# Optimization experiments

Measured on AMD Instinct MI355X. Metric: run time of the kernel, lower is better.

## Reference

```python
import jax, jax.numpy as jnp
import numpy as np

B, T, D = 8, 2048, 2048


def setup_inputs() -> dict:
    key = jax.random.key(0)
    ks = jax.random.split(key, 6)
    s = 1.0 / np.sqrt(D)
    return {
        "x": jax.random.normal(ks[0], (B, T, D), dtype=jnp.float32),
        "h_prev": jax.random.normal(ks[1], (B, D), dtype=jnp.float32),
        "Wz": jax.random.uniform(ks[2], (D, D), minval=-s, maxval=s, dtype=jnp.float32),
        "bz": jax.random.uniform(ks[3], (D,), minval=-s, maxval=s, dtype=jnp.float32),
        "Wh": jax.random.uniform(ks[4], (D, D), minval=-s, maxval=s, dtype=jnp.float32),
        "bh": jax.random.uniform(ks[5], (D,), minval=-s, maxval=s, dtype=jnp.float32),
    }


def reference(x, h_prev, Wz, bz, Wh, bh):
    # Batched projections over all timesteps (torch Linear: x @ W.T + b)
    z = jax.nn.sigmoid(jnp.einsum('btd,ed->bte', x, Wz) + bz)  # [B,T,D]
    h_tilde = jnp.einsum('btd,ed->bte', x, Wh) + bh            # [B,T,D]
    # Recurrence h_t = a_t * h_{t-1} + b_t as a parallel associative scan
    a = 1.0 - z
    b = z * h_tilde

    def combine(l, r):
        al, bl = l
        ar, br = r
        return (al * ar, ar * bl + br)

    a_cum, b_cum = jax.lax.associative_scan(combine, (a, b), axis=1)
    out = b_cum + a_cum * h_prev[:, None, :]  # add contribution of initial state
    return out, out[:, -1, :]
```

## Files before the change

### kernel.cpp

```cpp
#include <hip/hip_runtime.h>
#include <hip/hip_bf16.h>
#include <cstdint>

typedef __bf16 bf16_t;
typedef __attribute__((ext_vector_type(8))) __bf16 bf16x8;
typedef __attribute__((ext_vector_type(4))) __bf16 bf16x4;
typedef __attribute__((ext_vector_type(4))) float f32x4;

#define B_ 8
#define T_ 2048
#define D_ 2048
#define M_ (B_ * T_)
#define N2_ (2 * D_)
#define K_ D_
#define NT (K_ / 64)

#define NC 32
#define CHUNK (T_ / NC)

#define BAR() __builtin_amdgcn_s_barrier()
#define WAIT_LGKM0() asm volatile("s_waitcnt lgkmcnt(0)" ::: "memory")
#define WAIT_VM(n) asm volatile("s_waitcnt vmcnt(" #n ")" ::: "memory")


__global__ void conv_x_kernel(const float4* __restrict__ in, bf16x4* __restrict__ out, int n4) {
    int i = blockIdx.x * blockDim.x + threadIdx.x;
    if (i >= n4) return;
    float4 v = in[i];
    bf16x4 o = { (bf16_t)v.x, (bf16_t)v.y, (bf16_t)v.z, (bf16_t)v.w };
    out[i] = o;
}

__global__ void conv_w_kernel(const float4* __restrict__ Wz, const float4* __restrict__ Wh,
                              bf16x4* __restrict__ Wb, int n4, int d4) {
    int i = blockIdx.x * blockDim.x + threadIdx.x;
    if (i >= n4) return;
    int row = i / d4;
    int c = i - row * d4;
    float4 vz = Wz[i];
    float4 vh = Wh[i];
    bf16x4 oz = { (bf16_t)vz.x, (bf16_t)vz.y, (bf16_t)vz.z, (bf16_t)vz.w };
    bf16x4 oh = { (bf16_t)vh.x, (bf16_t)vh.y, (bf16_t)vh.z, (bf16_t)vh.w };
    Wb[(size_t)(2 * row) * d4 + c] = oz;
    Wb[(size_t)(2 * row + 1) * d4 + c] = oh;
}


__device__ __forceinline__ void gload_lds16(const bf16_t* g, char* l) {
    __builtin_amdgcn_global_load_lds(
        (__attribute__((address_space(1))) void*)(g),
        (__attribute__((address_space(3))) void*)(l), 16, 0, 0);
}


__global__ __launch_bounds__(512, 2) void gemm_fused(
    const bf16_t* __restrict__ Xb,
    const bf16_t* __restrict__ Wb,
    const float* __restrict__ bz, const float* __restrict__ bh,
    bf16_t* __restrict__ Aco,
    bf16_t* __restrict__ Bco)
{
    __shared__ __attribute__((aligned(16))) char lds[131072];

    const int t = threadIdx.x;
    const int wave = t >> 6, lane = t & 63;
    const int wr = wave >> 2, wc = wave & 3;
    const int fr = lane & 15, ln4 = lane >> 4;
    const int fr7 = fr & 7;
    const int bn0 = blockIdx.x * 256;
    const int bm0 = blockIdx.y * 256;

    const int l3 = lane >> 3, l7 = lane & 7;
    const int schunk = (l7 ^ l3) * 8;
    const int srow = wave * 8 + l3;

    const int csA[2] = { ((0 + ln4) ^ fr7) * 16, ((4 + ln4) ^ fr7) * 16 };
    const int rbaseA = wr * 16384 + fr * 128;
    const int rbaseB = wc * 8192 + fr * 128;

    auto stageA = [&](int buf, int h, int u) {
        const bf16_t* g = Xb + (size_t)(bm0 + h * 128 + srow) * K_ + u * 64 + schunk;
        char* l0 = lds + buf * 65536 + h * 16384 + wave * 1024;
        gload_lds16(g, l0);
        gload_lds16(g + (size_t)64 * K_, l0 + 8192);
    };
    auto stageB = [&](int buf, int h, int u) {
        const bf16_t* g = Wb + (size_t)(bn0 + h * 128 + srow) * K_ + u * 64 + schunk;
        char* l0 = lds + buf * 65536 + 32768 + h * 16384 + wave * 1024;
        gload_lds16(g, l0);
        gload_lds16(g + (size_t)64 * K_, l0 + 8192);
    };

#define RD_A(p, mi, kh) (*(const bf16x8*)(lds + (p) * 65536 + rbaseA + (mi) * 2048 + csA[kh]))
#define RD_B(p, ni, kh) (*(const bf16x8*)(lds + (p) * 65536 + 32768 + rbaseB + (ni) * 2048 + csA[kh]))

    f32x4 acc[8][4] = {};
    bf16x8 afr[4][2], bfr[4][2];

    stageA(0, 0, 0); stageA(0, 1, 0); stageB(0, 0, 0); stageB(0, 1, 0);
    stageA(1, 0, 1); stageA(1, 1, 1);
    WAIT_VM(4);
    BAR();

    for (int u = 0; u < NT; ++u) {
        const int p = u & 1;

#pragma unroll
        for (int mi = 0; mi < 4; ++mi)
#pragma unroll
            for (int kh = 0; kh < 2; ++kh)
                afr[mi][kh] = RD_A(p, mi, kh);
#pragma unroll
        for (int ni = 0; ni < 2; ++ni)
#pragma unroll
            for (int kh = 0; kh < 2; ++kh)
                bfr[ni][kh] = RD_B(p, ni, kh);
        if (u + 1 < NT) stageB(p ^ 1, 0, u + 1);
        BAR();
        __builtin_amdgcn_s_setprio(1);
#pragma unroll
        for (int mi = 0; mi < 4; ++mi)
#pragma unroll
            for (int ni = 0; ni < 2; ++ni)
#pragma unroll
                for (int kh = 0; kh < 2; ++kh)
                    acc[mi][ni] = __builtin_amdgcn_mfma_f32_16x16x32_bf16(
                        afr[mi][kh], bfr[ni][kh], acc[mi][ni], 0, 0, 0);
        __builtin_amdgcn_s_setprio(0);
        BAR();

#pragma unroll
        for (int ni = 2; ni < 4; ++ni)
#pragma unroll
            for (int kh = 0; kh < 2; ++kh)
                bfr[ni][kh] = RD_B(p, ni, kh);
        if (u + 1 < NT) stageB(p ^ 1, 1, u + 1);
        BAR();
        __builtin_amdgcn_s_setprio(1);
#pragma unroll
        for (int mi = 0; mi < 4; ++mi)
#pragma unroll
            for (int ni = 2; ni < 4; ++ni)
#pragma unroll
                for (int kh = 0; kh < 2; ++kh)
                    acc[mi][ni] = __builtin_amdgcn_mfma_f32_16x16x32_bf16(
                        afr[mi][kh], bfr[ni][kh], acc[mi][ni], 0, 0, 0);
        __builtin_amdgcn_s_setprio(0);
        BAR();

#pragma unroll
        for (int mi = 0; mi < 4; ++mi)
#pragma unroll
            for (int kh = 0; kh < 2; ++kh)
                afr[mi][kh] = RD_A(p, mi + 4, kh);
        WAIT_LGKM0();
        BAR();
        if (u + 2 < NT) stageA(p, 0, u + 2);
        __builtin_amdgcn_s_setprio(1);
#pragma unroll
        for (int mi = 0; mi < 4; ++mi)
#pragma unroll
            for (int ni = 0; ni < 2; ++ni)
#pragma unroll
                for (int kh = 0; kh < 2; ++kh)
                    acc[mi + 4][ni] = __builtin_amdgcn_mfma_f32_16x16x32_bf16(
                        afr[mi][kh], bfr[ni][kh], acc[mi + 4][ni], 0, 0, 0);
        __builtin_amdgcn_s_setprio(0);
        BAR();

        if (u + 2 < NT) stageA(p, 1, u + 2);
        __builtin_amdgcn_s_setprio(1);
#pragma unroll
        for (int mi = 0; mi < 4; ++mi)
#pragma unroll
            for (int ni = 2; ni < 4; ++ni)
#pragma unroll
                for (int kh = 0; kh < 2; ++kh)
                    acc[mi + 4][ni] = __builtin_amdgcn_mfma_f32_16x16x32_bf16(
                        afr[mi][kh], bfr[ni][kh], acc[mi + 4][ni], 0, 0, 0);
        __builtin_amdgcn_s_setprio(0);
        if (u < NT - 2)       { WAIT_VM(4); }
        else if (u == NT - 2) { WAIT_VM(0); }
        BAR();
    }

    float bzv[4], bhv[4];
#pragma unroll
    for (int ni = 0; ni < 4; ++ni) {
        int ch = (bn0 + wc * 64 + ni * 16 + fr) >> 1;
        bzv[ni] = bz[ch];
        bhv[ni] = bh[ch];
    }
#pragma unroll
    for (int mi = 0; mi < 8; ++mi) {
#pragma unroll
        for (int ni = 0; ni < 4; ++ni) {
#pragma unroll
            for (int q = 0; q < 4; ++q) {
                float v = acc[mi][ni][q];
                float other = __shfl_xor(v, 1);
                int m = bm0 + wr * 128 + mi * 16 + ln4 * 4 + q;
                int n2 = bn0 + wc * 64 + ni * 16 + fr;
                int ch = n2 >> 1;
                float zraw = (lane & 1) ? other : v;
                float z = 1.0f / (1.0f + __expf(-(zraw + bzv[ni])));
                if (lane & 1) {
                    Bco[(size_t)m * D_ + ch] = (bf16_t)(z * (v + bhv[ni]));
                } else {
                    Aco[(size_t)m * D_ + ch] = (bf16_t)(1.0f - z);
                }
            }
        }
    }
}


__global__ void scan_chunk_summary(const bf16_t* __restrict__ Aco, const bf16_t* __restrict__ Bco,
                                   float* __restrict__ cA, float* __restrict__ cB) {
    int d = blockIdx.x * blockDim.x + threadIdx.x;
    int c = blockIdx.y, bb = blockIdx.z;
    size_t base = ((size_t)bb * T_ + (size_t)c * CHUNK) * D_ + d;
    float A = 1.0f, Bv = 0.0f;
#pragma unroll 4
    for (int tt = 0; tt < CHUNK; ++tt) {
        float a = (float)Aco[base + (size_t)tt * D_];
        float b = (float)Bco[base + (size_t)tt * D_];
        A *= a;
        Bv = a * Bv + b;
    }
    size_t ci = ((size_t)bb * NC + c) * D_ + d;
    cA[ci] = A;
    cB[ci] = Bv;
}

__global__ void scan_carry(const float* __restrict__ cA, const float* __restrict__ cB,
                           const float* __restrict__ h_prev, float* __restrict__ carry) {
    int idx = blockIdx.x * blockDim.x + threadIdx.x;
    int bb = idx / D_, d = idx - bb * D_;
    float h = h_prev[idx];
    for (int c = 0; c < NC; ++c) {
        size_t ci = ((size_t)bb * NC + c) * D_ + d;
        carry[ci] = h;
        h = cA[ci] * h + cB[ci];
    }
}

__global__ void scan_apply(const bf16_t* __restrict__ Aco, const bf16_t* __restrict__ Bco,
                           const float* __restrict__ carry, float* __restrict__ out,
                           float* __restrict__ last) {
    int d = blockIdx.x * blockDim.x + threadIdx.x;
    int c = blockIdx.y, bb = blockIdx.z;
    size_t ci = ((size_t)bb * NC + c) * D_ + d;
    float h = carry[ci];
    size_t base = ((size_t)bb * T_ + (size_t)c * CHUNK) * D_ + d;
    for (int tt = 0; tt < CHUNK; ++tt) {
        float a = (float)Aco[base + (size_t)tt * D_];
        float b = (float)Bco[base + (size_t)tt * D_];
        h = a * h + b;
        out[base + (size_t)tt * D_] = h;
    }
    if (c == NC - 1) last[(size_t)bb * D_ + d] = h;
}


extern "C" void kernel_launch(void* const* d_in, const int* in_sizes, int n_in,
                              void* d_out, int out_size, void* d_ws, size_t ws_size,
                              hipStream_t stream) {
    const float* x      = (const float*)d_in[0];
    const float* h_prev = (const float*)d_in[1];
    const float* Wz     = (const float*)d_in[2];
    const float* bz     = (const float*)d_in[3];
    const float* Wh     = (const float*)d_in[4];
    const float* bh     = (const float*)d_in[5];

    float* out  = (float*)d_out;
    float* last = out + (size_t)M_ * D_;

    char* ws = (char*)d_ws;
    bf16_t* Xb  = (bf16_t*)ws;
    bf16_t* Wb  = (bf16_t*)(ws + (size_t)M_ * K_ * 2);
    bf16_t* Aco = (bf16_t*)((char*)Wb + (size_t)N2_ * K_ * 2);
    bf16_t* Bco = Aco + (size_t)M_ * D_;
    float*  cA  = (float*)((char*)Bco + (size_t)M_ * D_ * 2);
    float*  cB  = cA + (size_t)B_ * NC * D_;
    float*  carry = cB + (size_t)B_ * NC * D_;

    {
        int n4 = M_ * K_ / 4;
        conv_x_kernel<<<(n4 + 255) / 256, 256, 0, stream>>>((const float4*)x, (bf16x4*)Xb, n4);
    }
    {
        int n4 = D_ * D_ / 4;
        conv_w_kernel<<<(n4 + 255) / 256, 256, 0, stream>>>((const float4*)Wz, (const float4*)Wh,
                                                            (bf16x4*)Wb, n4, D_ / 4);
    }
    gemm_fused<<<dim3(N2_ / 256, M_ / 256), 512, 0, stream>>>(Xb, Wb, bz, bh, Aco, Bco);
    scan_chunk_summary<<<dim3(D_ / 256, NC, B_), 256, 0, stream>>>(Aco, Bco, cA, cB);
    scan_carry<<<(B_ * D_) / 256, 256, 0, stream>>>(cA, cB, h_prev, carry);
    scan_apply<<<dim3(D_ / 256, NC, B_), 256, 0, stream>>>(Aco, Bco, carry, out, last);
}
```

Before: 596.6 us.

## Interleave gate coefficients into packed words and fold carry scan into apply

The GEMM epilogue now writes the a and b coefficients as one packed 32-bit word (two bf16 values) per element instead of two separate bf16 arrays. Each scan kernel can then fetch both values with a single load. The separate scan_carry kernel is removed, and each apply block instead recomputes its starting carry by walking the earlier chunk summaries, which saves a launch and a round trip through memory at the cost of redundant serial work. Unroll factors in the scan loops are also raised.

```diff
diff --git a/kernel.cpp b/kernel.cpp
--- a/kernel.cpp
+++ b/kernel.cpp
@@ -1,6 +1,7 @@
 #include <hip/hip_runtime.h>
 #include <hip/hip_bf16.h>
 #include <cstdint>
+#include <cstring>
 
 typedef __bf16 bf16_t;
 typedef __attribute__((ext_vector_type(8))) __bf16 bf16x8;
@@ -21,6 +22,13 @@
 #define BAR() __builtin_amdgcn_s_barrier()
 #define WAIT_LGKM0() asm volatile("s_waitcnt lgkmcnt(0)" ::: "memory")
 #define WAIT_VM(n) asm volatile("s_waitcnt vmcnt(" #n ")" ::: "memory")
+
+__device__ __forceinline__ float bfbits_to_f(uint32_t u16) {
+    uint32_t u = u16 << 16;
+    float f;
+    memcpy(&f, &u, 4);
+    return f;
+}
 
 
 __global__ void conv_x_kernel(const float4* __restrict__ in, bf16x4* __restrict__ out, int n4) {
@@ -57,8 +65,7 @@
     const bf16_t* __restrict__ Xb,
     const bf16_t* __restrict__ Wb,
     const float* __restrict__ bz, const float* __restrict__ bh,
-    bf16_t* __restrict__ Aco,
-    bf16_t* __restrict__ Bco)
+    uint32_t* __restrict__ AB)
 {
     __shared__ __attribute__((aligned(16))) char lds[131072];
 
@@ -199,15 +206,16 @@
             for (int q = 0; q < 4; ++q) {
                 float v = acc[mi][ni][q];
                 float other = __shfl_xor(v, 1);
-                int m = bm0 + wr * 128 + mi * 16 + ln4 * 4 + q;
-                int n2 = bn0 + wc * 64 + ni * 16 + fr;
-                int ch = n2 >> 1;
-                float zraw = (lane & 1) ? other : v;
-                float z = 1.0f / (1.0f + __expf(-(zraw + bzv[ni])));
-                if (lane & 1) {
-                    Bco[(size_t)m * D_ + ch] = (bf16_t)(z * (v + bhv[ni]));
-                } else {
-                    Aco[(size_t)m * D_ + ch] = (bf16_t)(1.0f - z);
+                if (!(lane & 1)) {
+                    int m = bm0 + wr * 128 + mi * 16 + ln4 * 4 + q;
+                    int ch = (bn0 + wc * 64 + ni * 16 + fr) >> 1;
+                    float z = 1.0f / (1.0f + __expf(-(v + bzv[ni])));
+                    bf16_t av = (bf16_t)(1.0f - z);
+                    bf16_t bv = (bf16_t)(z * (other + bhv[ni]));
+                    uint16_t au, bu;
+                    memcpy(&au, &av, 2);
+                    memcpy(&bu, &bv, 2);
+                    AB[(size_t)m * D_ + ch] = ((uint32_t)bu << 16) | au;
                 }
             }
         }
@@ -215,16 +223,17 @@
 }
 
 
-__global__ void scan_chunk_summary(const bf16_t* __restrict__ Aco, const bf16_t* __restrict__ Bco,
+__global__ void scan_chunk_summary(const uint32_t* __restrict__ AB,
                                    float* __restrict__ cA, float* __restrict__ cB) {
     int d = blockIdx.x * blockDim.x + threadIdx.x;
     int c = blockIdx.y, bb = blockIdx.z;
     size_t base = ((size_t)bb * T_ + (size_t)c * CHUNK) * D_ + d;
     float A = 1.0f, Bv = 0.0f;
-#pragma unroll 4
+#pragma unroll 8
     for (int tt = 0; tt < CHUNK; ++tt) {
-        float a = (float)Aco[base + (size_t)tt * D_];
-        float b = (float)Bco[base + (size_t)tt * D_];
+        uint32_t w = AB[base + (size_t)tt * D_];
+        float a = bfbits_to_f(w & 0xffffu);
+        float b = bfbits_to_f(w >> 16);
         A *= a;
         Bv = a * Bv + b;
     }
@@ -233,29 +242,25 @@
     cB[ci] = Bv;
 }
 
-__global__ void scan_carry(const float* __restrict__ cA, const float* __restrict__ cB,
-                           const float* __restrict__ h_prev, float* __restrict__ carry) {
-    int idx = blockIdx.x * blockDim.x + threadIdx.x;
-    int bb = idx / D_, d = idx - bb * D_;
-    float h = h_prev[idx];
-    for (int c = 0; c < NC; ++c) {
-        size_t ci = ((size_t)bb * NC + c) * D_ + d;
-        carry[ci] = h;
-        h = cA[ci] * h + cB[ci];
-    }
-}
-
-__global__ void scan_apply(const bf16_t* __restrict__ Aco, const bf16_t* __restrict__ Bco,
-                           const float* __restrict__ carry, float* __restrict__ out,
+__global__ void scan_apply(const uint32_t* __restrict__ AB,
+                           const float* __restrict__ cA, const float* __restrict__ cB,
+                           const float* __restrict__ h_prev, float* __restrict__ out,
                            float* __restrict__ last) {
     int d = blockIdx.x * blockDim.x + threadIdx.x;
     int c = blockIdx.y, bb = blockIdx.z;
-    size_t ci = ((size_t)bb * NC + c) * D_ + d;
-    float h = carry[ci];
+
+    float h = h_prev[(size_t)bb * D_ + d];
+    size_t cbase = (size_t)bb * NC * D_ + d;
+#pragma unroll 4
+    for (int cc = 0; cc < c; ++cc)
+        h = cA[cbase + (size_t)cc * D_] * h + cB[cbase + (size_t)cc * D_];
+
     size_t base = ((size_t)bb * T_ + (size_t)c * CHUNK) * D_ + d;
+#pragma unroll 8
     for (int tt = 0; tt < CHUNK; ++tt) {
-        float a = (float)Aco[base + (size_t)tt * D_];
-        float b = (float)Bco[base + (size_t)tt * D_];
+        uint32_t w = AB[base + (size_t)tt * D_];
+        float a = bfbits_to_f(w & 0xffffu);
+        float b = bfbits_to_f(w >> 16);
         h = a * h + b;
         out[base + (size_t)tt * D_] = h;
     }
@@ -277,13 +282,11 @@
     float* last = out + (size_t)M_ * D_;
 
     char* ws = (char*)d_ws;
-    bf16_t* Xb  = (bf16_t*)ws;
-    bf16_t* Wb  = (bf16_t*)(ws + (size_t)M_ * K_ * 2);
-    bf16_t* Aco = (bf16_t*)((char*)Wb + (size_t)N2_ * K_ * 2);
-    bf16_t* Bco = Aco + (size_t)M_ * D_;
-    float*  cA  = (float*)((char*)Bco + (size_t)M_ * D_ * 2);
-    float*  cB  = cA + (size_t)B_ * NC * D_;
-    float*  carry = cB + (size_t)B_ * NC * D_;
+    bf16_t*   Xb = (bf16_t*)ws;
+    bf16_t*   Wb = (bf16_t*)(ws + (size_t)M_ * K_ * 2);
+    uint32_t* AB = (uint32_t*)((char*)Wb + (size_t)N2_ * K_ * 2);
+    float*    cA = (float*)((char*)AB + (size_t)M_ * D_ * 4);
+    float*    cB = cA + (size_t)B_ * NC * D_;
 
     {
         int n4 = M_ * K_ / 4;
@@ -294,8 +297,7 @@
         conv_w_kernel<<<(n4 + 255) / 256, 256, 0, stream>>>((const float4*)Wz, (const float4*)Wh,
                                                             (bf16x4*)Wb, n4, D_ / 4);
     }
-    gemm_fused<<<dim3(N2_ / 256, M_ / 256), 512, 0, stream>>>(Xb, Wb, bz, bh, Aco, Bco);
-    scan_chunk_summary<<<dim3(D_ / 256, NC, B_), 256, 0, stream>>>(Aco, Bco, cA, cB);
-    scan_carry<<<(B_ * D_) / 256, 256, 0, stream>>>(cA, cB, h_prev, carry);
-    scan_apply<<<dim3(D_ / 256, NC, B_), 256, 0, stream>>>(Aco, Bco, carry, out, last);
-}
+    gemm_fused<<<dim3(N2_ / 256, M_ / 256), 512, 0, stream>>>(Xb, Wb, bz, bh, AB);
+    scan_chunk_summary<<<dim3(D_ / 256, NC, B_), 256, 0, stream>>>(AB, cA, cB);
+    scan_apply<<<dim3(D_ / 256, NC, B_), 256, 0, stream>>>(AB, cA, cB, h_prev, out, last);
+}
```

Measured after the change: 612.0 us. 1.03x slower.
